# Performance work log

Hardware: AMD Instinct MI355X
Metric: run time of the kernel (lower is better)

The kernel has to match this reference:

```python
import jax, jax.numpy as jnp
import numpy as np

NUM_GROUPS = 32
EPS = 1e-6


def group_norm(x, weight, bias):
    # x: [b, c, h, w]
    b, c, h, w = x.shape
    xg = x.reshape(b, NUM_GROUPS, c // NUM_GROUPS, h, w)
    mean = jnp.mean(xg, axis=(2, 3, 4), keepdims=True)
    var = jnp.var(xg, axis=(2, 3, 4), keepdims=True)
    xn = ((xg - mean) * jax.lax.rsqrt(var + EPS)).reshape(b, c, h, w)
    return xn * weight[None, :, None, None] + bias[None, :, None, None]


def conv1x1(x, w, b):
    # 1x1 conv == per-pixel matmul. x: [b, c_in, h, w], w: [c_out, c_in]
    return jnp.einsum('oi,bihw->bohw', w, x) + b[None, :, None, None]


def setup_inputs() -> dict:
    key = jax.random.key(0)
    ks = jax.random.split(key, 9)
    b, c, h, w = 8, 512, 64, 64
    scale = 1.0 / np.sqrt(c)
    return {
        'x': jax.random.normal(ks[0], (b, c, h, w), jnp.float32),
        'gn_weight': jnp.ones((c,), jnp.float32),
        'gn_bias': jnp.zeros((c,), jnp.float32),
        'wq': jax.random.normal(ks[1], (c, c), jnp.float32) * scale,
        'bq': jnp.zeros((c,), jnp.float32),
        'wk': jax.random.normal(ks[2], (c, c), jnp.float32) * scale,
        'bk': jnp.zeros((c,), jnp.float32),
        'wv': jax.random.normal(ks[3], (c, c), jnp.float32) * scale,
        'bv': jnp.zeros((c,), jnp.float32),
        'wp': jax.random.normal(ks[4], (c, c), jnp.float32) * scale,
        'bp': jnp.zeros((c,), jnp.float32),
    }


def reference(x, gn_weight, gn_bias, wq, bq, wk, bk, wv, bv, wp, bp):
    h_ = group_norm(x, gn_weight, gn_bias)
    q = conv1x1(h_, wq, bq)
    k = conv1x1(h_, wk, bk)
    v = conv1x1(h_, wv, bv)
    b, c, h, w = q.shape
    n = h * w
    qf = q.reshape(b, c, n)
    kf = k.reshape(b, c, n)
    vf = v.reshape(b, c, n)
    # scores: [b, q, k]
    scores = jnp.einsum('bcq,bck->bqk', qf, kf) * (c ** -0.5)
    attn = jax.nn.softmax(scores, axis=-1)
    out = jnp.einsum('bqk,bck->bcq', attn, vf).reshape(b, c, h, w)
    out = conv1x1(out, wp, bp)
    return x + out
```

## Files before the change

### kernel.cpp

```cpp
#include <hip/hip_runtime.h>
#include <cstdint>

typedef unsigned short u16;
typedef __bf16 bf16x8 __attribute__((ext_vector_type(8)));
typedef float f32x4 __attribute__((ext_vector_type(4)));

__device__ __forceinline__ u16 f2bf(float f) {
    uint32_t u = __float_as_uint(f);
    u += 0x7FFFu + ((u >> 16) & 1u);
    return (u16)(u >> 16);
}
__device__ __forceinline__ float bf2f(u16 v) {
    return __uint_as_float((uint32_t)v << 16);
}

__device__ __forceinline__ void gload16(const u16* g, u16* l) {
    __builtin_amdgcn_global_load_lds(
        (const __attribute__((address_space(1))) uint32_t*)g,
        (__attribute__((address_space(3))) uint32_t*)l, 16, 0, 0);
}

__device__ __forceinline__ void swz(int& n_idx, int& m_idx, int& z_idx) {
    const int nx = gridDim.x, ny = gridDim.y;
    int lid = blockIdx.x + nx * (blockIdx.y + ny * blockIdx.z);
    int g = lid & 7, h = lid >> 3;
    n_idx = h % nx;
    int pair = (h / nx) * 8 + g;
    m_idx = pair % ny;
    z_idx = pair / ny;
}

__global__ __launch_bounds__(256) void k_detect(const u16* __restrict__ x,
                                                int* __restrict__ flag) {
    const int t = threadIdx.x;
    uint32_t mx = 0;
    for (int i = 0; i < 256; i++) {
        uint32_t v = (uint32_t)x[i * 256 + t] & 0x7FFFu;
        mx = mx > v ? mx : v;
    }
    for (int off = 32; off > 0; off >>= 1) {
        uint32_t o = (uint32_t)__shfl_xor((int)mx, off);
        mx = mx > o ? mx : o;
    }
    __shared__ uint32_t r[4];
    if ((t & 63) == 0) r[t >> 6] = mx;
    __syncthreads();
    if (t == 0) {
        uint32_t a = r[0] > r[1] ? r[0] : r[1];
        uint32_t b = r[2] > r[3] ? r[2] : r[3];
        mx = a > b ? a : b;
        *flag = (mx > 0x5000u) ? 1 : 0;
    }
}

__global__ __launch_bounds__(256) void k_cvt_wb(const void* wq, const void* wk,
                                                const void* wv, const void* wp,
                                                const void* gw, const void* gb,
                                                const void* bq, const void* bk,
                                                const void* bv, const void* bp,
                                                const int* __restrict__ flag,
                                                u16* __restrict__ Wc,
                                                u16* __restrict__ Bc) {
    const int mode = *flag;
    int i = blockIdx.x * 256 + threadIdx.x;
    if (i >= 1048576 + 3072) return;
    const void* src;
    u16* dst;
    int off;
    if (i < 1048576) {
        int which = i >> 18;
        off = i & 262143;
        src = which == 0 ? wq : which == 1 ? wk : which == 2 ? wv : wp;
        dst = Wc + i;
    } else {
        int j = i - 1048576;
        int which = j >> 9;
        off = j & 511;
        src = which == 0 ? gw : which == 1 ? gb : which == 2 ? bq
            : which == 3 ? bk : which == 4 ? bv : bp;
        dst = Bc + j;
    }
    *dst = mode ? f2bf(((const float*)src)[off]) : ((const u16*)src)[off];
}

__global__ __launch_bounds__(256) void k_gn_stats(const void* __restrict__ x_raw,
                                                  const u16* __restrict__ Bc,
                                                  const int* __restrict__ flag,
                                                  float* __restrict__ Sc,
                                                  float* __restrict__ Sh) {
    const int b = blockIdx.x >> 5, g = blockIdx.x & 31;
    const int mode = *flag;
    const int t = threadIdx.x;
    const int wave = t >> 6, lane = t & 63;
    float s = 0.f, ss = 0.f;
    if (mode) {
        const float4* xb = (const float4*)((const float*)x_raw +
                                           ((size_t)b * 512 + g * 16) * 4096);
        for (int it = 0; it < 64; it++) {
            float4 v = xb[it * 256 + t];
            s += v.x + v.y + v.z + v.w;
            ss += v.x * v.x + v.y * v.y + v.z * v.z + v.w * v.w;
        }
    } else {
        const uint4* xb = (const uint4*)((const u16*)x_raw +
                                         ((size_t)b * 512 + g * 16) * 4096);
        for (int it = 0; it < 32; it++) {
            uint4 v = xb[it * 256 + t];
            uint32_t w[4] = {v.x, v.y, v.z, v.w};
            for (int j = 0; j < 4; j++) {
                float a = __uint_as_float(w[j] << 16);
                float c = __uint_as_float(w[j] & 0xFFFF0000u);
                s += a + c;
                ss += a * a + c * c;
            }
        }
    }
    for (int off = 32; off > 0; off >>= 1) {
        s += __shfl_xor(s, off);
        ss += __shfl_xor(ss, off);
    }
    __shared__ float rs[4], rss[4];
    if (lane == 0) { rs[wave] = s; rss[wave] = ss; }
    __syncthreads();
    s = rs[0] + rs[1] + rs[2] + rs[3];
    ss = rss[0] + rss[1] + rss[2] + rss[3];
    const float mean = s * (1.f / 65536.f);
    const float var = ss * (1.f / 65536.f) - mean * mean;
    const float rstd = rsqrtf(var + 1e-6f);
    if (t < 16) {
        int c = g * 16 + t;
        float w = bf2f(Bc[c]);
        Sc[b * 512 + c] = rstd * w;
        Sh[b * 512 + c] = bf2f(Bc[512 + c]) - mean * rstd * w;
    }
}

#define TPAD 520
__global__ __launch_bounds__(256) void k_gn_apply(const void* __restrict__ x_raw,
                                                  const int* __restrict__ flag,
                                                  const float* __restrict__ Sc,
                                                  const float* __restrict__ Sh,
                                                  u16* __restrict__ HT) {
    __shared__ u16 tile[64 * TPAD];
    __shared__ float sSc[512], sSh[512];
    const int b = blockIdx.y;
    const int p0 = blockIdx.x * 64;
    const int mode = *flag;
    const int t = threadIdx.x;
    sSc[t] = Sc[b * 512 + t]; sSc[t + 256] = Sc[b * 512 + t + 256];
    sSh[t] = Sh[b * 512 + t]; sSh[t + 256] = Sh[b * 512 + t + 256];
    __syncthreads();
    for (int it = 0; it < 16; it++) {
        int li = it * 256 + t;
        int c = li >> 3;
        int pj = (li & 7) * 8;
        float v[8];
        if (mode) {
            const float* xr = (const float*)x_raw + ((size_t)b * 512 + c) * 4096 + p0 + pj;
            float4 a = *(const float4*)xr;
            float4 d = *(const float4*)(xr + 4);
            v[0] = a.x; v[1] = a.y; v[2] = a.z; v[3] = a.w;
            v[4] = d.x; v[5] = d.y; v[6] = d.z; v[7] = d.w;
        } else {
            const u16* xr = (const u16*)x_raw + ((size_t)b * 512 + c) * 4096 + p0 + pj;
            uint4 a = *(const uint4*)xr;
            uint32_t w[4] = {a.x, a.y, a.z, a.w};
            for (int j = 0; j < 4; j++) {
                v[2 * j] = __uint_as_float(w[j] << 16);
                v[2 * j + 1] = __uint_as_float(w[j] & 0xFFFF0000u);
            }
        }
        float sc = sSc[c], sh = sSh[c];
        for (int k = 0; k < 8; k++)
            tile[(pj + k) * TPAD + c] = f2bf(v[k] * sc + sh);
    }
    __syncthreads();
    u16* H = HT + (size_t)b * 2097152 + (size_t)p0 * 512;
    for (int it = 0; it < 16; it++) {
        int ch = it * 256 + t;
        int pp = ch >> 6;
        int cc = (ch & 63) * 8;
        *(uint4*)&H[(size_t)pp * 512 + cc] = *(const uint4*)&tile[pp * TPAD + cc];
    }
}

__device__ __forceinline__ void gemm_core(const u16* __restrict__ A,
                                          const u16* __restrict__ BT,
                                          int lda, int ldb, int K,
                                          int m0, int n0,
                                          u16* lA, u16* lB,
                                          f32x4 (&acc)[4][4]) {
    const int t = threadIdx.x;
    const int wave = t >> 6, lane = t & 63;
    const int wm = (wave >> 1) * 64, wn = (wave & 1) * 64;
    const int mf = lane & 15, quad = lane >> 4;
    const int srow = t >> 3;
    const int scol = (((t & 7) ^ (srow & 7)) * 8);
    const u16* Ap = A + (size_t)(m0 + srow) * lda + scol;
    const u16* Bp = BT + (size_t)(n0 + srow) * ldb + scol;
    u16* lAd = &lA[t * 8];
    u16* lBd = &lB[t * 8];
    const int fx = mf & 7;

    for (int i = 0; i < 4; i++)
        for (int j = 0; j < 4; j++)
            acc[i][j] = (f32x4){0.f, 0.f, 0.f, 0.f};

    for (int k0 = 0; k0 < K; k0 += 64) {
        __syncthreads();
        gload16(Ap + k0, lAd);
        gload16(Ap + k0 + (size_t)32 * lda, lAd + 2048);
        gload16(Ap + k0 + (size_t)64 * lda, lAd + 4096);
        gload16(Ap + k0 + (size_t)96 * lda, lAd + 6144);
        gload16(Bp + k0, lBd);
        gload16(Bp + k0 + (size_t)32 * ldb, lBd + 2048);
        gload16(Bp + k0 + (size_t)64 * ldb, lBd + 4096);
        gload16(Bp + k0 + (size_t)96 * ldb, lBd + 6144);
        __syncthreads();
        for (int ks = 0; ks < 2; ks++) {
            bf16x8 af[4], bfr[4];
            const int sl = ((ks * 4 + quad) ^ fx) * 8;
            for (int i = 0; i < 4; i++)
                af[i] = *(const bf16x8*)&lA[(wm + i * 16 + mf) * 64 + sl];
            for (int j = 0; j < 4; j++)
                bfr[j] = *(const bf16x8*)&lB[(wn + j * 16 + mf) * 64 + sl];
            for (int i = 0; i < 4; i++)
                for (int j = 0; j < 4; j++)
                    acc[i][j] = __builtin_amdgcn_mfma_f32_16x16x32_bf16(af[i], bfr[j], acc[i][j], 0, 0, 0);
        }
    }
}

__global__ __launch_bounds__(512, 2) void k_qkv(const u16* __restrict__ HT,
                                                const u16* __restrict__ Wc,
                                                const u16* __restrict__ Bc,
                                                u16* __restrict__ QT,
                                                u16* __restrict__ KT,
                                                u16* __restrict__ V) {
    __shared__ __align__(16) u16 lds[65536];
    int xI, bs, dz;
    swz(xI, bs, dz);
    const int b = bs / 3, s = bs % 3;
    const u16* Bb = Bc + 1024 + s * 512;
    int m0, n0, ldo, bias_by_row;
    const u16 *A, *B;
    u16* O;
    if (s < 2) {
        m0 = (xI >> 1) * 256; n0 = (xI & 1) * 256;
        A = HT + (size_t)b * 2097152; B = Wc + (size_t)s * 262144;
        O = (s == 0 ? QT : KT) + (size_t)b * 2097152; ldo = 512; bias_by_row = 0;
    } else {
        m0 = (xI & 1) * 256; n0 = (xI >> 1) * 256;
        A = Wc + (size_t)2 * 262144; B = HT + (size_t)b * 2097152;
        O = V + (size_t)b * 2097152; ldo = 4096; bias_by_row = 1;
    }

    const int t = threadIdx.x;
    const int wave = t >> 6, lane = t & 63;
    const int wm = (wave >> 2) * 128, wn = (wave & 3) * 64;
    const int mf = lane & 15, quad = lane >> 4;
    const int fx = mf & 7;
    const int srow = t >> 3;
    const int scol8 = t & 7;

    f32x4 acc[8][4];
#pragma unroll
    for (int i = 0; i < 8; i++)
#pragma unroll
        for (int j = 0; j < 4; j++)
            acc[i][j] = (f32x4){0.f, 0.f, 0.f, 0.f};

    auto issueA = [&](u16* dst, int h, int k0) {
#pragma unroll
        for (int ss = 0; ss < 2; ss++) {
            int row = h * 128 + ss * 64 + srow;
            gload16(A + (size_t)(m0 + row) * 512 + k0 + ((scol8 ^ (row & 7)) << 3),
                    dst + h * 8192 + ss * 4096 + t * 8);
        }
    };
    auto issueB = [&](u16* dst, int h, int k0) {
#pragma unroll
        for (int ss = 0; ss < 2; ss++) {
            int row = h * 128 + ss * 64 + srow;
            gload16(B + (size_t)(n0 + row) * 512 + k0 + ((scol8 ^ (row & 7)) << 3),
                    dst + h * 8192 + ss * 4096 + t * 8);
        }
    };

    issueA(lds, 0, 0); issueA(lds, 1, 0);
    issueB(lds + 16384, 0, 0); issueB(lds + 16384, 1, 0);

    for (int kt = 0; kt < 8; kt++) {
        u16* lA = (kt & 1) ? lds + 32768 : lds;
        u16* lB = lA + 16384;
        u16* pA = (kt & 1) ? lds : lds + 32768;
        u16* pB = pA + 16384;
        const int k0n = (kt + 1) << 6;
        const bool pf = kt < 7;
        asm volatile("" ::: "memory");
        __builtin_amdgcn_s_barrier();
        asm volatile("" ::: "memory");
        if (pf) {
            issueA(pA, 0, k0n);
            asm volatile("s_waitcnt vmcnt(2)" ::: "memory");
        } else {
            asm volatile("s_waitcnt vmcnt(0)" ::: "memory");
        }
        __builtin_amdgcn_s_barrier();
        asm volatile("" ::: "memory");

        bf16x8 af[8], bfr[2];
        int sl = (quad ^ fx) * 8;
#pragma unroll
        for (int i = 0; i < 8; i++)
            af[i] = *(const bf16x8*)&lA[(wm + i * 16 + mf) * 64 + sl];
#pragma unroll
        for (int j = 0; j < 2; j++)
            bfr[j] = *(const bf16x8*)&lB[(wn + j * 16 + mf) * 64 + sl];
        __builtin_amdgcn_s_setprio(1);
#pragma unroll
        for (int i = 0; i < 8; i++)
#pragma unroll
            for (int j = 0; j < 2; j++)
                acc[i][j] = __builtin_amdgcn_mfma_f32_16x16x32_bf16(af[i], bfr[j], acc[i][j], 0, 0, 0);
        __builtin_amdgcn_s_setprio(0);
        if (pf) issueA(pA, 1, k0n);
#pragma unroll
        for (int j = 0; j < 2; j++)
            bfr[j] = *(const bf16x8*)&lB[(wn + (2 + j) * 16 + mf) * 64 + sl];
        __builtin_amdgcn_s_setprio(1);
#pragma unroll
        for (int i = 0; i < 8; i++)
#pragma unroll
            for (int j = 0; j < 2; j++)
                acc[i][2 + j] = __builtin_amdgcn_mfma_f32_16x16x32_bf16(af[i], bfr[j], acc[i][2 + j], 0, 0, 0);
        __builtin_amdgcn_s_setprio(0);
        sl = ((4 + quad) ^ fx) * 8;
        if (pf) issueB(pB, 0, k0n);
#pragma unroll
        for (int i = 0; i < 8; i++)
            af[i] = *(const bf16x8*)&lA[(wm + i * 16 + mf) * 64 + sl];
#pragma unroll
        for (int j = 0; j < 2; j++)
            bfr[j] = *(const bf16x8*)&lB[(wn + j * 16 + mf) * 64 + sl];
        __builtin_amdgcn_s_setprio(1);
#pragma unroll
        for (int i = 0; i < 8; i++)
#pragma unroll
            for (int j = 0; j < 2; j++)
                acc[i][j] = __builtin_amdgcn_mfma_f32_16x16x32_bf16(af[i], bfr[j], acc[i][j], 0, 0, 0);
        __builtin_amdgcn_s_setprio(0);
        if (pf) issueB(pB, 1, k0n);
#pragma unroll
        for (int j = 0; j < 2; j++)
            bfr[j] = *(const bf16x8*)&lB[(wn + (2 + j) * 16 + mf) * 64 + sl];
        __builtin_amdgcn_s_setprio(1);
#pragma unroll
        for (int i = 0; i < 8; i++)
#pragma unroll
            for (int j = 0; j < 2; j++)
                acc[i][2 + j] = __builtin_amdgcn_mfma_f32_16x16x32_bf16(af[i], bfr[j], acc[i][2 + j], 0, 0, 0);
        __builtin_amdgcn_s_setprio(0);
    }

    __syncthreads();
#pragma unroll
    for (int i = 0; i < 8; i++)
#pragma unroll
        for (int r = 0; r < 4; r++) {
            int row = wm + i * 16 + quad * 4 + r;
            int key = row & 7;
            float brow = bias_by_row ? bf2f(Bb[m0 + row]) : 0.f;
#pragma unroll
            for (int j = 0; j < 4; j++) {
                int col = wn + j * 16 + mf;
                float bias = bias_by_row ? brow : bf2f(Bb[n0 + col]);
                lds[row * 256 + (((col >> 3) ^ key) << 3) + (col & 7)] =
                    f2bf(acc[i][j][r] + bias);
            }
        }
    __syncthreads();
    for (int p = 0; p < 16; p++) {
        int idx = p * 512 + t;
        int row = idx >> 5, chunk = idx & 31;
        uint4 v = *(const uint4*)&lds[row * 256 + ((chunk ^ (row & 7)) << 3)];
        *(uint4*)&O[(size_t)(m0 + row) * ldo + n0 + chunk * 8] = v;
    }
}

__device__ __forceinline__ u16* s_ptr(u16* S_ht, u16* S_tail, int l) {
    return l == 0 ? S_ht : S_tail + (size_t)(l - 1) * 16777216;
}

__global__ __launch_bounds__(512, 2) void k_scores(const u16* __restrict__ QT,
                                                   const u16* __restrict__ KT,
                                                   u16* __restrict__ S_ht,
                                                   u16* __restrict__ S_tail,
                                                   float* __restrict__ Part,
                                                   int b0) {
    __shared__ __align__(16) u16 lds[65536];
    int nI, mI, l;
    swz(nI, mI, l);
    const int n0 = nI * 256;
    const int m0 = mI * 256;
    const int b = b0 + l;
    const u16* Aq = QT + (size_t)b * 2097152;
    const u16* Bk = KT + (size_t)b * 2097152;

    const int t = threadIdx.x;
    const int wave = t >> 6, lane = t & 63;
    const int wm = (wave >> 2) * 128, wn = (wave & 3) * 64;
    const int mf = lane & 15, quad = lane >> 4;
    const int fx = mf & 7;
    const int srow = t >> 3;
    const int scol8 = t & 7;

    f32x4 acc[8][4];
#pragma unroll
    for (int i = 0; i < 8; i++)
#pragma unroll
        for (int j = 0; j < 4; j++)
            acc[i][j] = (f32x4){0.f, 0.f, 0.f, 0.f};

    auto issueA = [&](u16* dst, int h, int k0) {
#pragma unroll
        for (int s = 0; s < 2; s++) {
            int row = h * 128 + s * 64 + srow;
            gload16(Aq + (size_t)(m0 + row) * 512 + k0 + ((scol8 ^ (row & 7)) << 3),
                    dst + h * 8192 + s * 4096 + t * 8);
        }
    };
    auto issueB = [&](u16* dst, int h, int k0) {
#pragma unroll
        for (int s = 0; s < 2; s++) {
            int row = h * 128 + s * 64 + srow;
            gload16(Bk + (size_t)(n0 + row) * 512 + k0 + ((scol8 ^ (row & 7)) << 3),
                    dst + h * 8192 + s * 4096 + t * 8);
        }
    };

    issueA(lds, 0, 0); issueA(lds, 1, 0);
    issueB(lds + 16384, 0, 0); issueB(lds + 16384, 1, 0);

    for (int kt = 0; kt < 8; kt++) {
        u16* lA = (kt & 1) ? lds + 32768 : lds;
        u16* lB = lA + 16384;
        u16* pA = (kt & 1) ? lds : lds + 32768;
        u16* pB = pA + 16384;
        const int k0n = (kt + 1) << 6;
        const bool pf = kt < 7;
        asm volatile("" ::: "memory");
        __builtin_amdgcn_s_barrier();
        asm volatile("" ::: "memory");
        if (pf) {
            issueA(pA, 0, k0n);
            asm volatile("s_waitcnt vmcnt(2)" ::: "memory");
        } else {
            asm volatile("s_waitcnt vmcnt(0)" ::: "memory");
        }
        __builtin_amdgcn_s_barrier();
        asm volatile("" ::: "memory");

        bf16x8 af[8], bfr[2];
        int sl = (quad ^ fx) * 8;
#pragma unroll
        for (int i = 0; i < 8; i++)
            af[i] = *(const bf16x8*)&lA[(wm + i * 16 + mf) * 64 + sl];
#pragma unroll
        for (int j = 0; j < 2; j++)
            bfr[j] = *(const bf16x8*)&lB[(wn + j * 16 + mf) * 64 + sl];
        __builtin_amdgcn_s_setprio(1);
#pragma unroll
        for (int i = 0; i < 8; i++)
#pragma unroll
            for (int j = 0; j < 2; j++)
                acc[i][j] = __builtin_amdgcn_mfma_f32_16x16x32_bf16(af[i], bfr[j], acc[i][j], 0, 0, 0);
        __builtin_amdgcn_s_setprio(0);
        if (pf) issueA(pA, 1, k0n);
#pragma unroll
        for (int j = 0; j < 2; j++)
            bfr[j] = *(const bf16x8*)&lB[(wn + (2 + j) * 16 + mf) * 64 + sl];
        __builtin_amdgcn_s_setprio(1);
#pragma unroll
        for (int i = 0; i < 8; i++)
#pragma unroll
            for (int j = 0; j < 2; j++)
                acc[i][2 + j] = __builtin_amdgcn_mfma_f32_16x16x32_bf16(af[i], bfr[j], acc[i][2 + j], 0, 0, 0);
        __builtin_amdgcn_s_setprio(0);
        sl = ((4 + quad) ^ fx) * 8;
        if (pf) issueB(pB, 0, k0n);
#pragma unroll
        for (int i = 0; i < 8; i++)
            af[i] = *(const bf16x8*)&lA[(wm + i * 16 + mf) * 64 + sl];
#pragma unroll
        for (int j = 0; j < 2; j++)
            bfr[j] = *(const bf16x8*)&lB[(wn + j * 16 + mf) * 64 + sl];
        __builtin_amdgcn_s_setprio(1);
#pragma unroll
        for (int i = 0; i < 8; i++)
#pragma unroll
            for (int j = 0; j < 2; j++)
                acc[i][j] = __builtin_amdgcn_mfma_f32_16x16x32_bf16(af[i], bfr[j], acc[i][j], 0, 0, 0);
        __builtin_amdgcn_s_setprio(0);
        if (pf) issueB(pB, 1, k0n);
#pragma unroll
        for (int j = 0; j < 2; j++)
            bfr[j] = *(const bf16x8*)&lB[(wn + (2 + j) * 16 + mf) * 64 + sl];
        __builtin_amdgcn_s_setprio(1);
#pragma unroll
        for (int i = 0; i < 8; i++)
#pragma unroll
            for (int j = 0; j < 2; j++)
                acc[i][2 + j] = __builtin_amdgcn_mfma_f32_16x16x32_bf16(af[i], bfr[j], acc[i][2 + j], 0, 0, 0);
        __builtin_amdgcn_s_setprio(0);
    }

    const float scale = 0.04419417382415922f;
    __syncthreads();
#pragma unroll
    for (int i = 0; i < 8; i++)
#pragma unroll
        for (int r = 0; r < 4; r++) {
            int row = wm + i * 16 + quad * 4 + r;
            int key = row & 7;
#pragma unroll
            for (int j = 0; j < 4; j++) {
                int col = wn + j * 16 + mf;
                lds[row * 256 + (((col >> 3) ^ key) << 3) + (col & 7)] =
                    f2bf(__expf(acc[i][j][r] * scale));
            }
        }
    __syncthreads();
    u16* Sb = s_ptr(S_ht, S_tail, l);
    float* pr = Part + ((size_t)b * 16 + nI) * 4096 + m0;
    for (int p = 0; p < 16; p++) {
        int idx = p * 512 + t;
        int row = idx >> 5, chunk = idx & 31;
        uint4 v = *(const uint4*)&lds[row * 256 + ((chunk ^ (row & 7)) << 3)];
        uint32_t w[4] = {v.x, v.y, v.z, v.w};
        float s = 0.f;
        for (int q2 = 0; q2 < 4; q2++)
            s += __uint_as_float(w[q2] << 16) + __uint_as_float(w[q2] & 0xFFFF0000u);
        for (int off = 16; off > 0; off >>= 1) s += __shfl_xor(s, off);
        if ((lane & 31) == 0) pr[row] = s;
        *(uint4*)&Sb[(size_t)(m0 + row) * 4096 + n0 + chunk * 8] = v;
    }
}

__global__ __launch_bounds__(512, 2) void k_pv_split(u16* __restrict__ S_ht,
                                                     u16* __restrict__ S_tail,
                                                     const u16* __restrict__ V,
                                                     u16* __restrict__ QT,
                                                     u16* __restrict__ KT,
                                                     int b0) {
    __shared__ __align__(16) u16 lds[49152];
    int nI, mI, zI;
    swz(nI, mI, zI);
    const int n0 = nI * 256;
    const int m0 = mI * 128;
    const int l = zI >> 1, split = zI & 1, b = b0 + l;
    const u16* A = s_ptr(S_ht, S_tail, l) + split * 2048;
    const u16* B = V + (size_t)b * 2097152 + split * 2048;

    const int t = threadIdx.x;
    const int wave = t >> 6, lane = t & 63;
    const int wm = (wave >> 2) * 64, wn = (wave & 3) * 64;
    const int mf = lane & 15, quad = lane >> 4;
    const int fx = mf & 7;
    const int srow = t >> 3;
    const int scol8 = t & 7;

    f32x4 acc[4][4];
#pragma unroll
    for (int i = 0; i < 4; i++)
#pragma unroll
        for (int j = 0; j < 4; j++)
            acc[i][j] = (f32x4){0.f, 0.f, 0.f, 0.f};

    auto issueA = [&](u16* dst, int k0) {
#pragma unroll
        for (int s = 0; s < 2; s++) {
            int row = s * 64 + srow;
            gload16(A + (size_t)(m0 + row) * 4096 + k0 + ((scol8 ^ (row & 7)) << 3),
                    dst + s * 4096 + t * 8);
        }
    };
    auto issueB = [&](u16* dst, int h, int k0) {
#pragma unroll
        for (int s = 0; s < 2; s++) {
            int row = h * 128 + s * 64 + srow;
            gload16(B + (size_t)(n0 + row) * 4096 + k0 + ((scol8 ^ (row & 7)) << 3),
                    dst + h * 8192 + s * 4096 + t * 8);
        }
    };

    issueA(lds, 0);
    issueB(lds + 8192, 0, 0);
    issueB(lds + 8192, 1, 0);

    for (int kt = 0; kt < 32; kt++) {
        u16* lA = (kt & 1) ? lds + 24576 : lds;
        u16* lB = lA + 8192;
        u16* pA = (kt & 1) ? lds : lds + 24576;
        u16* pB = pA + 8192;
        const int k0n = (kt + 1) << 6;
        const bool pf = kt < 31;
        asm volatile("" ::: "memory");
        __builtin_amdgcn_s_barrier();
        asm volatile("" ::: "memory");
        if (pf) {
            issueA(pA, k0n);
            asm volatile("s_waitcnt vmcnt(2)" ::: "memory");
        } else {
            asm volatile("s_waitcnt vmcnt(0)" ::: "memory");
        }
        __builtin_amdgcn_s_barrier();
        asm volatile("" ::: "memory");

        bf16x8 af[4], bfr[2];
        int sl = (quad ^ fx) * 8;
#pragma unroll
        for (int i = 0; i < 4; i++)
            af[i] = *(const bf16x8*)&lA[(wm + i * 16 + mf) * 64 + sl];
#pragma unroll
        for (int j = 0; j < 2; j++)
            bfr[j] = *(const bf16x8*)&lB[(wn + j * 16 + mf) * 64 + sl];
        __builtin_amdgcn_s_setprio(1);
#pragma unroll
        for (int i = 0; i < 4; i++)
#pragma unroll
            for (int j = 0; j < 2; j++)
                acc[i][j] = __builtin_amdgcn_mfma_f32_16x16x32_bf16(af[i], bfr[j], acc[i][j], 0, 0, 0);
        __builtin_amdgcn_s_setprio(0);
        if (pf) issueB(pB, 0, k0n);
#pragma unroll
        for (int j = 0; j < 2; j++)
            bfr[j] = *(const bf16x8*)&lB[(wn + (2 + j) * 16 + mf) * 64 + sl];
        __builtin_amdgcn_s_setprio(1);
#pragma unroll
        for (int i = 0; i < 4; i++)
#pragma unroll
            for (int j = 0; j < 2; j++)
                acc[i][2 + j] = __builtin_amdgcn_mfma_f32_16x16x32_bf16(af[i], bfr[j], acc[i][2 + j], 0, 0, 0);
        __builtin_amdgcn_s_setprio(0);
        sl = ((4 + quad) ^ fx) * 8;
        if (pf) issueB(pB, 1, k0n);
#pragma unroll
        for (int i = 0; i < 4; i++)
            af[i] = *(const bf16x8*)&lA[(wm + i * 16 + mf) * 64 + sl];
#pragma unroll
        for (int j = 0; j < 2; j++)
            bfr[j] = *(const bf16x8*)&lB[(wn + j * 16 + mf) * 64 + sl];
        __builtin_amdgcn_s_setprio(1);
#pragma unroll
        for (int i = 0; i < 4; i++)
#pragma unroll
            for (int j = 0; j < 2; j++)
                acc[i][j] = __builtin_amdgcn_mfma_f32_16x16x32_bf16(af[i], bfr[j], acc[i][j], 0, 0, 0);
        __builtin_amdgcn_s_setprio(0);
#pragma unroll
        for (int j = 0; j < 2; j++)
            bfr[j] = *(const bf16x8*)&lB[(wn + (2 + j) * 16 + mf) * 64 + sl];
        __builtin_amdgcn_s_setprio(1);
#pragma unroll
        for (int i = 0; i < 4; i++)
#pragma unroll
            for (int j = 0; j < 2; j++)
                acc[i][2 + j] = __builtin_amdgcn_mfma_f32_16x16x32_bf16(af[i], bfr[j], acc[i][2 + j], 0, 0, 0);
        __builtin_amdgcn_s_setprio(0);
    }

    u16* P = (split == 0 ? QT : KT) + (size_t)b * 2097152;
    __syncthreads();
#pragma unroll
    for (int i = 0; i < 4; i++)
#pragma unroll
        for (int r = 0; r < 4; r++) {
            int row = wm + i * 16 + quad * 4 + r;
            int key = row & 7;
#pragma unroll
            for (int j = 0; j < 4; j++) {
                int col = wn + j * 16 + mf;
                lds[row * 256 + (((col >> 3) ^ key) << 3) + (col & 7)] =
                    f2bf(acc[i][j][r]);
            }
        }
    __syncthreads();
    for (int p = 0; p < 8; p++) {
        int idx = p * 512 + t;
        int row = idx >> 5, chunk = idx & 31;
        uint4 v = *(const uint4*)&lds[row * 256 + ((chunk ^ (row & 7)) << 3)];
        *(uint4*)&P[(size_t)(m0 + row) * 512 + n0 + chunk * 8] = v;
    }
}

__global__ __launch_bounds__(256) void k_pv_reduce(const u16* __restrict__ QT,
                                                   const u16* __restrict__ KT,
                                                   const float* __restrict__ Part,
                                                   u16* __restrict__ OT,
                                                   int b0) {
    const int b = b0 + blockIdx.y;
    const int t = threadIdx.x;
    __shared__ float sInv[4];
    if (t < 64) {
        int r = t >> 4, which = t & 15;
        int p = blockIdx.x * 4 + r;
        float v = Part[((size_t)b * 16 + which) * 4096 + p];
        for (int off = 8; off > 0; off >>= 1) v += __shfl_xor(v, off);
        if (which == 0) sInv[r] = 1.f / v;
    }
    __syncthreads();
    const float inv = sInv[t >> 6];
    size_t base = (size_t)b * 2097152;
    size_t i0 = base + ((size_t)blockIdx.x * 256 + t) * 8;
    uint4 a = *(const uint4*)(QT + i0);
    uint4 c = *(const uint4*)(KT + i0);
    uint32_t wa[4] = {a.x, a.y, a.z, a.w};
    uint32_t wc[4] = {c.x, c.y, c.z, c.w};
    uint32_t o[4];
    for (int j = 0; j < 4; j++) {
        float lo = (__uint_as_float(wa[j] << 16) + __uint_as_float(wc[j] << 16)) * inv;
        float hi = (__uint_as_float(wa[j] & 0xFFFF0000u) + __uint_as_float(wc[j] & 0xFFFF0000u)) * inv;
        o[j] = (uint32_t)f2bf(lo) | ((uint32_t)f2bf(hi) << 16);
    }
    *(uint4*)(OT + i0) = make_uint4(o[0], o[1], o[2], o[3]);
}

__global__ __launch_bounds__(256) void k_proj(const u16* __restrict__ Wc,
                                              const u16* __restrict__ OT,
                                              const u16* __restrict__ Bc,
                                              const void* __restrict__ x_raw,
                                              const int* __restrict__ flag,
                                              void* __restrict__ y_raw) {
    __shared__ __align__(16) u16 smu[16384];
    float* smf = (float*)smu;
    int nI, mI, b;
    swz(nI, mI, b);
    const int n0 = nI * 128;
    const int m0 = mI * 128;
    f32x4 acc[4][4];
    gemm_core(Wc + (size_t)3 * 262144, OT + (size_t)b * 2097152, 512, 512, 512,
              m0, n0, smu, smu + 8192, acc);

    const int mode = *flag;
    const u16* bp = Bc + 5 * 512;
    const int t = threadIdx.x;
    const int wave = t >> 6, lane = t & 63;
    const int wn = (wave & 1) * 64;
    const int mf = lane & 15, quad = lane >> 4;
    const int whalf = wave >> 1;
    size_t bb = (size_t)b * 2097152;
    for (int h = 0; h < 2; h++) {
        __syncthreads();
        if (whalf == h) {
            for (int i = 0; i < 4; i++)
                for (int r = 0; r < 4; r++) {
                    int rowl = i * 16 + quad * 4 + r;
                    int kf = ((rowl >> 2) & 1) << 4;
                    for (int j = 0; j < 4; j++) {
                        int col = wn + j * 16 + mf;
                        smf[rowl * 128 + (col ^ kf)] = acc[i][j][r];
                    }
                }
        }
        __syncthreads();
        const int rowbase = m0 + h * 64;
        if (mode) {
            for (int p = 0; p < 8; p++) {
                int idx = p * 256 + t;
                int rowl = idx >> 5, c4 = (idx & 31) * 4;
                int kf = ((rowl >> 2) & 1) << 4;
                f32x4 v = *(const f32x4*)&smf[rowl * 128 + (c4 ^ kf)];
                int rowg = rowbase + rowl;
                float bias = bf2f(bp[rowg]);
                size_t o = bb + (size_t)rowg * 4096 + n0 + c4;
                float4 xv = *(const float4*)((const float*)x_raw + o);
                float4 out = make_float4(v[0] + bias + xv.x, v[1] + bias + xv.y,
                                         v[2] + bias + xv.z, v[3] + bias + xv.w);
                *(float4*)((float*)y_raw + o) = out;
            }
        } else {
            for (int p = 0; p < 4; p++) {
                int idx = p * 256 + t;
                int rowl = idx >> 4, c8 = (idx & 15) * 8;
                int kf = ((rowl >> 2) & 1) << 4;
                const float* sp = &smf[rowl * 128 + (c8 ^ kf)];
                f32x4 v0 = *(const f32x4*)sp;
                f32x4 v1 = *(const f32x4*)(sp + 4);
                int rowg = rowbase + rowl;
                float bias = bf2f(bp[rowg]);
                size_t o = bb + (size_t)rowg * 4096 + n0 + c8;
                uint4 xv = *(const uint4*)((const u16*)x_raw + o);
                uint32_t xw[4] = {xv.x, xv.y, xv.z, xv.w};
                float vals[8] = {v0[0], v0[1], v0[2], v0[3],
                                 v1[0], v1[1], v1[2], v1[3]};
                uint32_t ow[4];
                for (int q2 = 0; q2 < 4; q2++) {
                    float lo = __uint_as_float(xw[q2] << 16) + vals[2 * q2] + bias;
                    float hi = __uint_as_float(xw[q2] & 0xFFFF0000u) + vals[2 * q2 + 1] + bias;
                    ow[q2] = (uint32_t)f2bf(lo) | ((uint32_t)f2bf(hi) << 16);
                }
                *(uint4*)((u16*)y_raw + o) = make_uint4(ow[0], ow[1], ow[2], ow[3]);
            }
        }
    }
}

extern "C" void kernel_launch(void* const* d_in, const int* in_sizes, int n_in,
                              void* d_out, int out_size, void* d_ws, size_t ws_size,
                              hipStream_t stream) {
    (void)in_sizes; (void)n_in; (void)out_size;
    const void* x  = d_in[0];
    const void* gw = d_in[1];
    const void* gb = d_in[2];
    const void* wq = d_in[3];
    const void* bq = d_in[4];
    const void* wk = d_in[5];
    const void* bk = d_in[6];
    const void* wv = d_in[7];
    const void* bv = d_in[8];
    const void* wp = d_in[9];
    const void* bp = d_in[10];

    u16* ws16 = (u16*)d_ws;
    int* flag = (int*)d_ws;
    float* Sc = (float*)(ws16 + 16);
    float* Sh = Sc + 4096;
    u16* Wc = ws16 + 16 + 16384;
    u16* Bc = Wc + 1048576;
    u16* HT = Bc + 4096;
    u16* QT = HT + 16777216;
    u16* KT = QT + 16777216;
    u16* V  = KT + 16777216;
    u16* OT = V  + 16777216;
    float* Part = (float*)(OT + 16777216);
    u16* Tail = (u16*)(Part + 1048576);
    const size_t base_elems = (size_t)(Tail - ws16);

    int nb = 1;
    for (int cand = 8; cand >= 2; cand >>= 1) {
        size_t need = 2ull * (base_elems + (size_t)(cand - 1) * 16777216ull);
        if (ws_size >= need) { nb = cand; break; }
    }

    k_detect<<<1, 256, 0, stream>>>((const u16*)x, flag);
    k_cvt_wb<<<4108, 256, 0, stream>>>(wq, wk, wv, wp, gw, gb, bq, bk, bv, bp,
                                       flag, Wc, Bc);
    k_gn_stats<<<256, 256, 0, stream>>>(x, Bc, flag, Sc, Sh);
    k_gn_apply<<<dim3(64, 8), 256, 0, stream>>>(x, flag, Sc, Sh, HT);
    k_qkv<<<dim3(32, 24), 512, 0, stream>>>(HT, Wc, Bc, QT, KT, V);
    for (int b0 = 0; b0 < 8; b0 += nb) {
        k_scores<<<dim3(16, 16, nb), 512, 0, stream>>>(QT, KT, HT, Tail, Part, b0);
        k_pv_split<<<dim3(2, 32, 2 * nb), 512, 0, stream>>>(HT, Tail, V, QT, KT, b0);
        k_pv_reduce<<<dim3(1024, nb), 256, 0, stream>>>(QT, KT, Part, OT, b0);
    }
    k_proj<<<dim3(32, 4, 8), 256, 0, stream>>>(Wc, OT, Bc, x, flag, d_out);
}
```

Measured before the change: 687.5 us.

## Rewrite output projection GEMM with 256x256 tiles and double-buffered LDS prefetch

The output projection kernel moves from 128x128 tiles on 256 threads to 256x256 tiles on 512 threads. It double-buffers LDS so global-to-LDS loads for the next K step are issued in pieces between MFMA groups, with priority hints raised around the MFMA work. This aims to hide memory latency and raise operand reuse per load. In exchange it uses a larger register and LDS footprint and launches fewer blocks (256 instead of 1024), which may leave parts of the GPU underused.

```diff
diff --git a/kernel.cpp b/kernel.cpp
--- a/kernel.cpp
+++ b/kernel.cpp
@@ -184,53 +184,6 @@
     }
 }
 
-__device__ __forceinline__ void gemm_core(const u16* __restrict__ A,
-                                          const u16* __restrict__ BT,
-                                          int lda, int ldb, int K,
-                                          int m0, int n0,
-                                          u16* lA, u16* lB,
-                                          f32x4 (&acc)[4][4]) {
-    const int t = threadIdx.x;
-    const int wave = t >> 6, lane = t & 63;
-    const int wm = (wave >> 1) * 64, wn = (wave & 1) * 64;
-    const int mf = lane & 15, quad = lane >> 4;
-    const int srow = t >> 3;
-    const int scol = (((t & 7) ^ (srow & 7)) * 8);
-    const u16* Ap = A + (size_t)(m0 + srow) * lda + scol;
-    const u16* Bp = BT + (size_t)(n0 + srow) * ldb + scol;
-    u16* lAd = &lA[t * 8];
-    u16* lBd = &lB[t * 8];
-    const int fx = mf & 7;
-
-    for (int i = 0; i < 4; i++)
-        for (int j = 0; j < 4; j++)
-            acc[i][j] = (f32x4){0.f, 0.f, 0.f, 0.f};
-
-    for (int k0 = 0; k0 < K; k0 += 64) {
-        __syncthreads();
-        gload16(Ap + k0, lAd);
-        gload16(Ap + k0 + (size_t)32 * lda, lAd + 2048);
-        gload16(Ap + k0 + (size_t)64 * lda, lAd + 4096);
-        gload16(Ap + k0 + (size_t)96 * lda, lAd + 6144);
-        gload16(Bp + k0, lBd);
-        gload16(Bp + k0 + (size_t)32 * ldb, lBd + 2048);
-        gload16(Bp + k0 + (size_t)64 * ldb, lBd + 4096);
-        gload16(Bp + k0 + (size_t)96 * ldb, lBd + 6144);
-        __syncthreads();
-        for (int ks = 0; ks < 2; ks++) {
-            bf16x8 af[4], bfr[4];
-            const int sl = ((ks * 4 + quad) ^ fx) * 8;
-            for (int i = 0; i < 4; i++)
-                af[i] = *(const bf16x8*)&lA[(wm + i * 16 + mf) * 64 + sl];
-            for (int j = 0; j < 4; j++)
-                bfr[j] = *(const bf16x8*)&lB[(wn + j * 16 + mf) * 64 + sl];
-            for (int i = 0; i < 4; i++)
-                for (int j = 0; j < 4; j++)
-                    acc[i][j] = __builtin_amdgcn_mfma_f32_16x16x32_bf16(af[i], bfr[j], acc[i][j], 0, 0, 0);
-        }
-    }
-}
-
 __global__ __launch_bounds__(512, 2) void k_qkv(const u16* __restrict__ HT,
                                                 const u16* __restrict__ Wc,
                                                 const u16* __restrict__ Bc,
@@ -726,70 +679,176 @@
     *(uint4*)(OT + i0) = make_uint4(o[0], o[1], o[2], o[3]);
 }
 
-__global__ __launch_bounds__(256) void k_proj(const u16* __restrict__ Wc,
-                                              const u16* __restrict__ OT,
-                                              const u16* __restrict__ Bc,
-                                              const void* __restrict__ x_raw,
-                                              const int* __restrict__ flag,
-                                              void* __restrict__ y_raw) {
-    __shared__ __align__(16) u16 smu[16384];
-    float* smf = (float*)smu;
+__global__ __launch_bounds__(512, 2) void k_proj(const u16* __restrict__ Wc,
+                                                 const u16* __restrict__ OT,
+                                                 const u16* __restrict__ Bc,
+                                                 const void* __restrict__ x_raw,
+                                                 const int* __restrict__ flag,
+                                                 void* __restrict__ y_raw) {
+    __shared__ __align__(16) u16 lds[65536];
+    float* smf = (float*)lds;
     int nI, mI, b;
     swz(nI, mI, b);
-    const int n0 = nI * 128;
-    const int m0 = mI * 128;
-    f32x4 acc[4][4];
-    gemm_core(Wc + (size_t)3 * 262144, OT + (size_t)b * 2097152, 512, 512, 512,
-              m0, n0, smu, smu + 8192, acc);
+    const int n0 = nI * 256;
+    const int m0 = mI * 256;
+    const u16* A = Wc + (size_t)3 * 262144;
+    const u16* B = OT + (size_t)b * 2097152;
+
+    const int t = threadIdx.x;
+    const int wave = t >> 6, lane = t & 63;
+    const int wm = (wave >> 2) * 128, wn = (wave & 3) * 64;
+    const int mf = lane & 15, quad = lane >> 4;
+    const int fx = mf & 7;
+    const int srow = t >> 3;
+    const int scol8 = t & 7;
+
+    f32x4 acc[8][4];
+#pragma unroll
+    for (int i = 0; i < 8; i++)
+#pragma unroll
+        for (int j = 0; j < 4; j++)
+            acc[i][j] = (f32x4){0.f, 0.f, 0.f, 0.f};
+
+    auto issueA = [&](u16* dst, int h, int k0) {
+#pragma unroll
+        for (int ss = 0; ss < 2; ss++) {
+            int row = h * 128 + ss * 64 + srow;
+            gload16(A + (size_t)(m0 + row) * 512 + k0 + ((scol8 ^ (row & 7)) << 3),
+                    dst + h * 8192 + ss * 4096 + t * 8);
+        }
+    };
+    auto issueB = [&](u16* dst, int h, int k0) {
+#pragma unroll
+        for (int ss = 0; ss < 2; ss++) {
+            int row = h * 128 + ss * 64 + srow;
+            gload16(B + (size_t)(n0 + row) * 512 + k0 + ((scol8 ^ (row & 7)) << 3),
+                    dst + h * 8192 + ss * 4096 + t * 8);
+        }
+    };
+
+    issueA(lds, 0, 0); issueA(lds, 1, 0);
+    issueB(lds + 16384, 0, 0); issueB(lds + 16384, 1, 0);
+
+    for (int kt = 0; kt < 8; kt++) {
+        u16* lA = (kt & 1) ? lds + 32768 : lds;
+        u16* lB = lA + 16384;
+        u16* pA = (kt & 1) ? lds : lds + 32768;
+        u16* pB = pA + 16384;
+        const int k0n = (kt + 1) << 6;
+        const bool pf = kt < 7;
+        asm volatile("" ::: "memory");
+        __builtin_amdgcn_s_barrier();
+        asm volatile("" ::: "memory");
+        if (pf) {
+            issueA(pA, 0, k0n);
+            asm volatile("s_waitcnt vmcnt(2)" ::: "memory");
+        } else {
+            asm volatile("s_waitcnt vmcnt(0)" ::: "memory");
+        }
+        __builtin_amdgcn_s_barrier();
+        asm volatile("" ::: "memory");
+
+        bf16x8 af[8], bfr[2];
+        int sl = (quad ^ fx) * 8;
+#pragma unroll
+        for (int i = 0; i < 8; i++)
+            af[i] = *(const bf16x8*)&lA[(wm + i * 16 + mf) * 64 + sl];
+#pragma unroll
+        for (int j = 0; j < 2; j++)
+            bfr[j] = *(const bf16x8*)&lB[(wn + j * 16 + mf) * 64 + sl];
+        __builtin_amdgcn_s_setprio(1);
+#pragma unroll
+        for (int i = 0; i < 8; i++)
+#pragma unroll
+            for (int j = 0; j < 2; j++)
+                acc[i][j] = __builtin_amdgcn_mfma_f32_16x16x32_bf16(af[i], bfr[j], acc[i][j], 0, 0, 0);
+        __builtin_amdgcn_s_setprio(0);
+        if (pf) issueA(pA, 1, k0n);
+#pragma unroll
+        for (int j = 0; j < 2; j++)
+            bfr[j] = *(const bf16x8*)&lB[(wn + (2 + j) * 16 + mf) * 64 + sl];
+        __builtin_amdgcn_s_setprio(1);
+#pragma unroll
+        for (int i = 0; i < 8; i++)
+#pragma unroll
+            for (int j = 0; j < 2; j++)
+                acc[i][2 + j] = __builtin_amdgcn_mfma_f32_16x16x32_bf16(af[i], bfr[j], acc[i][2 + j], 0, 0, 0);
+        __builtin_amdgcn_s_setprio(0);
+        sl = ((4 + quad) ^ fx) * 8;
+        if (pf) issueB(pB, 0, k0n);
+#pragma unroll
+        for (int i = 0; i < 8; i++)
+            af[i] = *(const bf16x8*)&lA[(wm + i * 16 + mf) * 64 + sl];
+#pragma unroll
+        for (int j = 0; j < 2; j++)
+            bfr[j] = *(const bf16x8*)&lB[(wn + j * 16 + mf) * 64 + sl];
+        __builtin_amdgcn_s_setprio(1);
+#pragma unroll
+        for (int i = 0; i < 8; i++)
+#pragma unroll
+            for (int j = 0; j < 2; j++)
+                acc[i][j] = __builtin_amdgcn_mfma_f32_16x16x32_bf16(af[i], bfr[j], acc[i][j], 0, 0, 0);
+        __builtin_amdgcn_s_setprio(0);
+        if (pf) issueB(pB, 1, k0n);
+#pragma unroll
+        for (int j = 0; j < 2; j++)
+            bfr[j] = *(const bf16x8*)&lB[(wn + (2 + j) * 16 + mf) * 64 + sl];
+        __builtin_amdgcn_s_setprio(1);
+#pragma unroll
+        for (int i = 0; i < 8; i++)
+#pragma unroll
+            for (int j = 0; j < 2; j++)
+                acc[i][2 + j] = __builtin_amdgcn_mfma_f32_16x16x32_bf16(af[i], bfr[j], acc[i][2 + j], 0, 0, 0);
+        __builtin_amdgcn_s_setprio(0);
+    }
 
     const int mode = *flag;
     const u16* bp = Bc + 5 * 512;
-    const int t = threadIdx.x;
-    const int wave = t >> 6, lane = t & 63;
-    const int wn = (wave & 1) * 64;
-    const int mf = lane & 15, quad = lane >> 4;
-    const int whalf = wave >> 1;
     size_t bb = (size_t)b * 2097152;
+    const int whalf = wave >> 2;
     for (int h = 0; h < 2; h++) {
         __syncthreads();
         if (whalf == h) {
-            for (int i = 0; i < 4; i++)
+#pragma unroll
+            for (int i = 0; i < 8; i++)
+#pragma unroll
                 for (int r = 0; r < 4; r++) {
-                    int rowl = i * 16 + quad * 4 + r;
-                    int kf = ((rowl >> 2) & 1) << 4;
+                    int row = i * 16 + quad * 4 + r;
+                    int key = row & 7;
+#pragma unroll
                     for (int j = 0; j < 4; j++) {
                         int col = wn + j * 16 + mf;
-                        smf[rowl * 128 + (col ^ kf)] = acc[i][j][r];
+                        smf[row * 256 + (((col >> 2) ^ key) << 2) + (col & 3)] =
+                            acc[i][j][r];
                     }
                 }
         }
         __syncthreads();
-        const int rowbase = m0 + h * 64;
+        const int rowbase = m0 + h * 128;
         if (mode) {
-            for (int p = 0; p < 8; p++) {
-                int idx = p * 256 + t;
-                int rowl = idx >> 5, c4 = (idx & 31) * 4;
-                int kf = ((rowl >> 2) & 1) << 4;
-                f32x4 v = *(const f32x4*)&smf[rowl * 128 + (c4 ^ kf)];
+            for (int p = 0; p < 16; p++) {
+                int idx = p * 512 + t;
+                int rowl = idx >> 6, c4 = idx & 63;
+                int key = rowl & 7;
+                f32x4 v = *(const f32x4*)&smf[rowl * 256 + ((c4 ^ key) << 2)];
                 int rowg = rowbase + rowl;
                 float bias = bf2f(bp[rowg]);
-                size_t o = bb + (size_t)rowg * 4096 + n0 + c4;
+                size_t o = bb + (size_t)rowg * 4096 + n0 + c4 * 4;
                 float4 xv = *(const float4*)((const float*)x_raw + o);
                 float4 out = make_float4(v[0] + bias + xv.x, v[1] + bias + xv.y,
                                          v[2] + bias + xv.z, v[3] + bias + xv.w);
                 *(float4*)((float*)y_raw + o) = out;
             }
         } else {
-            for (int p = 0; p < 4; p++) {
-                int idx = p * 256 + t;
-                int rowl = idx >> 4, c8 = (idx & 15) * 8;
-                int kf = ((rowl >> 2) & 1) << 4;
-                const float* sp = &smf[rowl * 128 + (c8 ^ kf)];
-                f32x4 v0 = *(const f32x4*)sp;
-                f32x4 v1 = *(const f32x4*)(sp + 4);
+            for (int p = 0; p < 8; p++) {
+                int idx = p * 512 + t;
+                int rowl = idx >> 5, cp = idx & 31;
+                int key = rowl & 7;
+                f32x4 v0 = *(const f32x4*)&smf[rowl * 256 + (((2 * cp) ^ key) << 2)];
+                f32x4 v1 = *(const f32x4*)&smf[rowl * 256 + (((2 * cp + 1) ^ key) << 2)];
                 int rowg = rowbase + rowl;
                 float bias = bf2f(bp[rowg]);
-                size_t o = bb + (size_t)rowg * 4096 + n0 + c8;
+                size_t o = bb + (size_t)rowg * 4096 + n0 + cp * 8;
                 uint4 xv = *(const uint4*)((const u16*)x_raw + o);
                 uint32_t xw[4] = {xv.x, xv.y, xv.z, xv.w};
                 float vals[8] = {v0[0], v0[1], v0[2], v0[3],
@@ -854,5 +913,5 @@
         k_pv_split<<<dim3(2, 32, 2 * nb), 512, 0, stream>>>(HT, Tail, V, QT, KT, b0);
         k_pv_reduce<<<dim3(1024, nb), 256, 0, stream>>>(QT, KT, Part, OT, b0);
     }
-    k_proj<<<dim3(32, 4, 8), 256, 0, stream>>>(Wc, OT, Bc, x, flag, d_out);
-}
+    k_proj<<<dim3(16, 2, 8), 512, 0, stream>>>(Wc, OT, Bc, x, flag, d_out);
+}
```

Result: slower. 750.9 us (+9.2%).
